# Optimization experiments

Measured on AMD Instinct MI355X. Metric: run time of the kernel, lower is better.

## Reference

```python
import jax, jax.numpy as jnp
import numpy as np

N_NODES = 100000
N_GRAPHS = 256
HIDDEN = 64
IN_DIM = 512


def gcn_conv(x, edge_index, W, b, n_nodes):
    """PyG GCNConv: out = D^{-1/2} (A+I) D^{-1/2} (x W) + b."""
    h = x @ W  # [N, H] -- transform first (as PyG does), messages are small
    src = jnp.concatenate([edge_index[0], jnp.arange(n_nodes)])  # add self loops
    dst = jnp.concatenate([edge_index[1], jnp.arange(n_nodes)])
    ones = jnp.ones(src.shape[0], dtype=h.dtype)
    deg = jax.ops.segment_sum(ones, dst, num_segments=n_nodes)
    dinv = jnp.where(deg > 0, jax.lax.rsqrt(deg), 0.0)
    norm = dinv[src] * dinv[dst]  # [E+N]
    msg = h[src] * norm[:, None]  # gather + scale
    out = jax.ops.segment_sum(msg, dst, num_segments=n_nodes)  # scatter-add
    return out + b


def global_mean_pool(x, batch, num_graphs):
    s = jax.ops.segment_sum(x, batch, num_segments=num_graphs)
    cnt = jax.ops.segment_sum(jnp.ones(x.shape[0], dtype=x.dtype), batch,
                              num_segments=num_graphs)
    return s / jnp.maximum(cnt, 1.0)[:, None]


def setup_inputs() -> dict:
    key = jax.random.key(0)
    ks = jax.random.split(key, 9)
    x = jax.random.normal(ks[0], (N_NODES, IN_DIM), dtype=jnp.float32)
    edge_index = jax.random.randint(ks[1], (2, 1600000), 0, N_NODES, dtype=jnp.int64) \
        if jax.config.jax_enable_x64 else jax.random.randint(ks[1], (2, 1600000), 0, N_NODES).astype(jnp.int32)
    batch = jnp.sort(jax.random.randint(ks[2], (N_NODES,), 0, N_GRAPHS))
    sc1 = 1.0 / np.sqrt(IN_DIM)
    sc2 = 1.0 / np.sqrt(HIDDEN)
    W1 = jax.random.uniform(ks[3], (IN_DIM, HIDDEN), minval=-sc1, maxval=sc1, dtype=jnp.float32)
    b1 = jnp.zeros((HIDDEN,), dtype=jnp.float32)
    W2 = jax.random.uniform(ks[4], (HIDDEN, HIDDEN), minval=-sc2, maxval=sc2, dtype=jnp.float32)
    b2 = jnp.zeros((HIDDEN,), dtype=jnp.float32)
    Wfc = jax.random.uniform(ks[5], (HIDDEN, 1), minval=-sc2, maxval=sc2, dtype=jnp.float32)
    bfc = jnp.zeros((1,), dtype=jnp.float32)
    return {"x": x, "edge_index": edge_index, "batch": batch,
            "W1": W1, "b1": b1, "W2": W2, "b2": b2, "Wfc": Wfc, "bfc": bfc}


def reference(x, edge_index, batch, W1, b1, W2, b2, Wfc, bfc):
    n = x.shape[0]
    h = jax.nn.relu(gcn_conv(x, edge_index, W1, b1, n))
    h = jax.nn.relu(gcn_conv(h, edge_index, W2, b2, n))
    g = global_mean_pool(h, batch, N_GRAPHS)  # [G, H]
    out = g @ Wfc + bfc  # [G, 1]
    return out.squeeze(-1)
```

## Files before the change

### kernel.cpp

```cpp
#include <hip/hip_runtime.h>

#define HIDDEN 64
#define IN_DIM 512
#define CAP 4096
#define NB_MAX 1024

typedef short v8s __attribute__((ext_vector_type(8)));
typedef float v4f __attribute__((ext_vector_type(4)));

static __device__ __forceinline__ unsigned short f2bf(float f) {
    unsigned int u = __float_as_uint(f);
    u = (u + 0x7FFF + ((u >> 16) & 1)) >> 16;
    return (unsigned short)u;
}
static __device__ __forceinline__ float bf2f(unsigned short u) {
    return __uint_as_float(((unsigned int)u) << 16);
}
static __device__ __forceinline__ float bflo(unsigned u) { return __uint_as_float(u << 16); }
static __device__ __forceinline__ float bfhi(unsigned u) { return __uint_as_float(u & 0xffff0000u); }

__global__ void k_init(int* cursor, float* gsum, int* gcnt) {
    int i = blockIdx.x * 256 + threadIdx.x;
    if (i < NB_MAX) cursor[i] = 0;
    if (i < 256) { gsum[i] = 0.f; gcnt[i] = 0; }
}

__launch_bounds__(256)
__global__ void k_bin(const int* __restrict__ src, const int* __restrict__ dst,
                      int* cursor, unsigned* __restrict__ bucket_data, int n_edges) {
    __shared__ unsigned words[4096];
    __shared__ unsigned short binsh[4096];
    __shared__ int hist[NB_MAX];
    __shared__ int base[NB_MAX];
    const int tid = threadIdx.x;
    const int e0 = blockIdx.x * 4096;
    for (int i = tid; i < NB_MAX; i += 256) hist[i] = 0;
    __syncthreads();
    for (int i = tid; i < 4096; i += 256) {
        int e = e0 + i;
        if (e < n_edges) {
            int d = dst[e], s = src[e];
            words[i] = ((unsigned)s << 7) | (unsigned)(d & 127);
            int b = d >> 7;
            binsh[i] = (unsigned short)b;
            atomicAdd(&hist[b], 1);
        } else binsh[i] = 0xFFFFu;
    }
    __syncthreads();
    for (int b = tid; b < NB_MAX; b += 256) {
        int c = hist[b];
        base[b] = c ? atomicAdd(&cursor[b], c) : 0;
        hist[b] = 0;
    }
    __syncthreads();
    for (int i = tid; i < 4096; i += 256) {
        unsigned short b = binsh[i];
        if (b != 0xFFFFu) {
            int slot = atomicAdd(&hist[b], 1);
            int p = base[b] + slot;
            if (p < CAP) bucket_data[(size_t)b * CAP + p] = words[i];
        }
    }
}

__launch_bounds__(256)
__global__ void k_bexc(const int* __restrict__ cursor, int* __restrict__ bucket_base,
                       int* __restrict__ row_start, int n_nodes, int nbuck) {
    __shared__ int wsum[4];
    const int t = threadIdx.x, lane = t & 63, w = t >> 6;
    int v[4], s = 0;
#pragma unroll
    for (int k = 0; k < 4; ++k) {
        int i = t * 4 + k;
        int c = (i < nbuck) ? cursor[i] : 0;
        if (c > CAP) c = CAP;
        v[k] = s; s += c;
    }
    int inc = s;
#pragma unroll
    for (int off = 1; off < 64; off <<= 1) {
        int u = __shfl_up(inc, off, 64);
        if (lane >= off) inc += u;
    }
    if (lane == 63) wsum[w] = inc;
    __syncthreads();
    int cross = 0;
    for (int i = 0; i < w; ++i) cross += wsum[i];
    int b0 = cross + inc - s;
#pragma unroll
    for (int k = 0; k < 4; ++k) {
        int i = t * 4 + k;
        if (i < NB_MAX) bucket_base[i] = b0 + v[k];
    }
    if (t == 255) row_start[n_nodes] = cross + inc;
}

__launch_bounds__(256)
__global__ void k_csr(const unsigned* __restrict__ bucket_data, const int* __restrict__ cursor,
                      const int* __restrict__ bucket_base,
                      int* __restrict__ row_start, int* __restrict__ csr,
                      float* __restrict__ dinv, int n_nodes) {
    __shared__ unsigned words[CAP];
    __shared__ int cnt[128];
    __shared__ int loff[128];
    __shared__ int cur[128];
    __shared__ int w0sum;
    const int tid = threadIdx.x, bin = blockIdx.x, n0 = bin << 7;
    int c = cursor[bin]; if (c > CAP) c = CAP;
    const unsigned* bd = bucket_data + (size_t)bin * CAP;
    for (int i = tid; i < c; i += 256) words[i] = bd[i];
    if (tid < 128) { cnt[tid] = 0; cur[tid] = 0; }
    __syncthreads();
    for (int i = tid; i < c; i += 256) atomicAdd(&cnt[words[i] & 127], 1);
    __syncthreads();
    int val = 0, inc = 0;
    if (tid < 128) {
        const int lane = tid & 63;
        val = cnt[tid];
        inc = val;
#pragma unroll
        for (int off = 1; off < 64; off <<= 1) {
            int u = __shfl_up(inc, off, 64);
            if (lane >= off) inc += u;
        }
        if (tid == 63) w0sum = inc;
    }
    __syncthreads();
    if (tid < 128) {
        int excl = inc - val + ((tid >= 64) ? w0sum : 0);
        loff[tid] = excl;
        int n = n0 + tid;
        if (n < n_nodes) {
            row_start[n] = bucket_base[bin] + excl;
            dinv[n] = rsqrtf((float)(val + 1));
        }
    }
    __syncthreads();
    const int gbase = bucket_base[bin];
    for (int i = tid; i < c; i += 256) {
        unsigned wd = words[i];
        int d = wd & 127;
        int slot = atomicAdd(&cur[d], 1);
        csr[gbase + loff[d] + slot] = (int)(wd >> 7);
    }
}

__global__ void k_prep(const float* __restrict__ W1, const float* __restrict__ W2,
                       unsigned short* __restrict__ Wt, unsigned short* __restrict__ Wt2) {
    int idx = blockIdx.x * 256 + threadIdx.x;
    if (idx < HIDDEN * IN_DIM) {
        int n = idx >> 9, k = idx & 511;
        Wt[(size_t)n * 512 + k] = f2bf(W1[(size_t)k * 64 + n]);
    } else {
        int j = idx - HIDDEN * IN_DIM;
        int n = j >> 6, k = j & 63;
        Wt2[(size_t)n * 64 + k] = f2bf(W2[(size_t)k * 64 + n]);
    }
}

__launch_bounds__(256)
__global__ void k_gemm1m(const float* __restrict__ x, const unsigned short* __restrict__ Wt,
                         const float* __restrict__ dinv, unsigned short* __restrict__ s1,
                         int n_nodes) {
    __shared__ __align__(16) unsigned short lX[64 * 136];
    __shared__ __align__(16) unsigned short lW[64 * 136];
    const int tid  = threadIdx.x;
    const int lane = tid & 63;
    const int w    = tid >> 6;
    const int quad = lane >> 4;
    const int m16  = lane & 15;
    const int row0 = blockIdx.x * 64;

    v4f acc[4];
#pragma unroll
    for (int b = 0; b < 4; ++b) acc[b] = (v4f){0.f, 0.f, 0.f, 0.f};

    for (int kc = 0; kc < IN_DIM; kc += 128) {
        __syncthreads();
#pragma unroll
        for (int i = 0; i < 8; ++i) {
            int fidx = tid + i * 256;
            int r  = fidx >> 5;
            int c4 = fidx & 31;
            int gr = row0 + r;
            float4 v = make_float4(0.f, 0.f, 0.f, 0.f);
            if (gr < n_nodes) v = ((const float4*)(x + (size_t)gr * IN_DIM + kc))[c4];
            ushort4 u = make_ushort4(f2bf(v.x), f2bf(v.y), f2bf(v.z), f2bf(v.w));
            *(ushort4*)(lX + r * 136 + c4 * 4) = u;
        }
#pragma unroll
        for (int i = 0; i < 4; ++i) {
            int idx = tid + i * 256;
            int n  = idx >> 4;
            int c8 = idx & 15;
            uint4 u = *(const uint4*)(Wt + (size_t)n * 512 + kc + c8 * 8);
            *(uint4*)(lW + n * 136 + c8 * 8) = u;
        }
        __syncthreads();
#pragma unroll
        for (int kk = 0; kk < 128; kk += 32) {
            v8s a = *(const v8s*)(lX + (w * 16 + m16) * 136 + kk + quad * 8);
#pragma unroll
            for (int b = 0; b < 4; ++b) {
                v8s bb = *(const v8s*)(lW + (b * 16 + m16) * 136 + kk + quad * 8);
                acc[b] = __builtin_amdgcn_mfma_f32_16x16x32_bf16(a, bb, acc[b], 0, 0, 0);
            }
        }
    }
    __syncthreads();
    float* lC = (float*)lX;
#pragma unroll
    for (int b = 0; b < 4; ++b)
#pragma unroll
        for (int r = 0; r < 4; ++r) {
            int rowt = w * 16 + quad * 4 + r;
            lC[rowt * 65 + b * 16 + m16] = acc[b][r];
        }
    __syncthreads();
#pragma unroll
    for (int i = 0; i < 2; ++i) {
        int base = i * 2048 + tid * 8;
        int r = base >> 6;
        int c = base & 63;
        int gr = row0 + r;
        if (gr < n_nodes) {
            float d = dinv[gr];
            const float* p = lC + r * 65 + c;
            unsigned p0 = (unsigned)f2bf(p[0] * d) | ((unsigned)f2bf(p[1] * d) << 16);
            unsigned p1 = (unsigned)f2bf(p[2] * d) | ((unsigned)f2bf(p[3] * d) << 16);
            unsigned p2 = (unsigned)f2bf(p[4] * d) | ((unsigned)f2bf(p[5] * d) << 16);
            unsigned p3 = (unsigned)f2bf(p[6] * d) | ((unsigned)f2bf(p[7] * d) << 16);
            *(uint4*)(s1 + (size_t)gr * 64 + c) = make_uint4(p0, p1, p2, p3);
        }
    }
}

#define NPW 4

__launch_bounds__(256)
__global__ void k_agg1(const unsigned short* __restrict__ sin, const int* __restrict__ row_start,
                       const int* __restrict__ csr, const float* __restrict__ dinv,
                       float* __restrict__ tout, int n_nodes) {
    const int tid = threadIdx.x;
    const int lane = tid & 63;
    const int wave = tid >> 6;
    const int g = lane >> 4;
    const int l = lane & 15;
    const int n0 = (blockIdx.x * 4 + wave) * NPW;
    if (n0 >= n_nodes) return;

    int rs_nxt = row_start[n0];
    int idx_nxt = csr[rs_nxt + lane];
    uint2 us_nxt = *(const uint2*)(sin + (size_t)n0 * HIDDEN + l * 4);

    for (int i = 0; i < NPW; ++i) {
        int n = n0 + i;
        if (n >= n_nodes) break;
        const int rs = rs_nxt;
        const int re = row_start[n + 1];
        const int idx = idx_nxt;
        const uint2 uself = us_nxt;
        if (i + 1 < NPW && n + 1 < n_nodes) {
            rs_nxt = re;
            idx_nxt = csr[re + lane];
            us_nxt = *(const uint2*)(sin + (size_t)(n + 1) * HIDDEN + l * 4);
        }

        float4 acc = make_float4(0.f, 0.f, 0.f, 0.f);
        int m0 = re - rs; if (m0 > 64) m0 = 64;
        int mq = (m0 + 3) >> 2;
#pragma unroll 4
        for (int jq = 0; jq < mq; ++jq) {
            int myj = jq * 4 + g;
            int cm = myj < m0 ? myj : 0;
            int a = __shfl(idx, cm, 64);
            uint2 u = *(const uint2*)(sin + (size_t)a * HIDDEN + l * 4);
            if (myj < m0) {
                acc.x += bflo(u.x); acc.y += bfhi(u.x);
                acc.z += bflo(u.y); acc.w += bfhi(u.y);
            }
        }
        if (__builtin_expect(re - rs > 64, 0)) {
            for (int base = rs + 64; base < re; base += 64) {
                int idx2 = csr[base + lane];
                int m = re - base; if (m > 64) m = 64;
                int mq2 = (m + 3) >> 2;
#pragma unroll 4
                for (int jq = 0; jq < mq2; ++jq) {
                    int myj = jq * 4 + g;
                    int cm = myj < m ? myj : 0;
                    int a = __shfl(idx2, cm, 64);
                    uint2 u = *(const uint2*)(sin + (size_t)a * HIDDEN + l * 4);
                    if (myj < m) {
                        acc.x += bflo(u.x); acc.y += bfhi(u.x);
                        acc.z += bflo(u.y); acc.w += bfhi(u.y);
                    }
                }
            }
        }
        acc.x += __shfl_xor(acc.x, 16, 64); acc.y += __shfl_xor(acc.y, 16, 64);
        acc.z += __shfl_xor(acc.z, 16, 64); acc.w += __shfl_xor(acc.w, 16, 64);
        acc.x += __shfl_xor(acc.x, 32, 64); acc.y += __shfl_xor(acc.y, 32, 64);
        acc.z += __shfl_xor(acc.z, 32, 64); acc.w += __shfl_xor(acc.w, 32, 64);
        acc.x += bflo(uself.x); acc.y += bfhi(uself.x);
        acc.z += bflo(uself.y); acc.w += bfhi(uself.y);
        float d = dinv[n];
        if (g == 0) {
            float4 t4 = make_float4(d * acc.x, d * acc.y, d * acc.z, d * acc.w);
            *(float4*)(tout + (size_t)n * HIDDEN + l * 4) = t4;
        }
    }
}

__launch_bounds__(256)
__global__ void k_gemm2m(const float* __restrict__ tin, const unsigned short* __restrict__ Wt2,
                         const float* __restrict__ b1, const float* __restrict__ dinv,
                         unsigned short* __restrict__ sout, int n_nodes) {
    __shared__ __align__(16) unsigned short lX[64 * 136];
    __shared__ __align__(16) unsigned short lW[64 * 72];
    const int tid  = threadIdx.x;
    const int lane = tid & 63;
    const int w    = tid >> 6;
    const int quad = lane >> 4;
    const int m16  = lane & 15;
    const int row0 = blockIdx.x * 64;

#pragma unroll
    for (int i = 0; i < 4; ++i) {
        int fidx = tid + i * 256;
        int r  = fidx >> 4;
        int c4 = fidx & 15;
        int gr = row0 + r;
        float4 v = make_float4(0.f, 0.f, 0.f, 0.f);
        if (gr < n_nodes) v = ((const float4*)(tin + (size_t)gr * HIDDEN))[c4];
        float4 bb = ((const float4*)b1)[c4];
        v.x = fmaxf(v.x + bb.x, 0.f);
        v.y = fmaxf(v.y + bb.y, 0.f);
        v.z = fmaxf(v.z + bb.z, 0.f);
        v.w = fmaxf(v.w + bb.w, 0.f);
        ushort4 u = make_ushort4(f2bf(v.x), f2bf(v.y), f2bf(v.z), f2bf(v.w));
        *(ushort4*)(lX + r * 72 + c4 * 4) = u;
    }
#pragma unroll
    for (int i = 0; i < 2; ++i) {
        int idx = tid + i * 256;
        int n  = idx >> 3;
        int c8 = idx & 7;
        uint4 u = *(const uint4*)(Wt2 + (size_t)n * 64 + c8 * 8);
        *(uint4*)(lW + n * 72 + c8 * 8) = u;
    }
    __syncthreads();
    v4f acc[4];
#pragma unroll
    for (int b = 0; b < 4; ++b) acc[b] = (v4f){0.f, 0.f, 0.f, 0.f};
#pragma unroll
    for (int kk = 0; kk < 64; kk += 32) {
        v8s a = *(const v8s*)(lX + (w * 16 + m16) * 72 + kk + quad * 8);
#pragma unroll
        for (int b = 0; b < 4; ++b) {
            v8s bb = *(const v8s*)(lW + (b * 16 + m16) * 72 + kk + quad * 8);
            acc[b] = __builtin_amdgcn_mfma_f32_16x16x32_bf16(a, bb, acc[b], 0, 0, 0);
        }
    }
    __syncthreads();
    float* lC = (float*)lX;
#pragma unroll
    for (int b = 0; b < 4; ++b)
#pragma unroll
        for (int r = 0; r < 4; ++r) {
            int rowt = w * 16 + quad * 4 + r;
            lC[rowt * 65 + b * 16 + m16] = acc[b][r];
        }
    __syncthreads();
#pragma unroll
    for (int i = 0; i < 2; ++i) {
        int base = i * 2048 + tid * 8;
        int r = base >> 6;
        int c = base & 63;
        int gr = row0 + r;
        if (gr < n_nodes) {
            float d = dinv[gr];
            const float* p = lC + r * 65 + c;
            unsigned p0 = (unsigned)f2bf(p[0] * d) | ((unsigned)f2bf(p[1] * d) << 16);
            unsigned p1 = (unsigned)f2bf(p[2] * d) | ((unsigned)f2bf(p[3] * d) << 16);
            unsigned p2 = (unsigned)f2bf(p[4] * d) | ((unsigned)f2bf(p[5] * d) << 16);
            unsigned p3 = (unsigned)f2bf(p[6] * d) | ((unsigned)f2bf(p[7] * d) << 16);
            *(uint4*)(sout + (size_t)gr * 64 + c) = make_uint4(p0, p1, p2, p3);
        }
    }
}

__launch_bounds__(256)
__global__ void k_layer2pool(const unsigned short* __restrict__ sin, const int* __restrict__ row_start,
                             const int* __restrict__ csr, const float* __restrict__ b2,
                             const float* __restrict__ dinv, const float* __restrict__ Wfc,
                             const int* __restrict__ batch,
                             float* gsum, int* gcnt, int n_nodes) {
    __shared__ float lsum[256];
    __shared__ int   lcnt[256];
    const int tid = threadIdx.x;
    lsum[tid] = 0.f; lcnt[tid] = 0;
    __syncthreads();
    const int lane = tid & 63;
    const int wave = tid >> 6;
    const int g = lane >> 4;
    const int l = lane & 15;
    const float4 b4  = ((const float4*)b2)[l];
    const float4 wf4 = ((const float4*)Wfc)[l];
    const int n0 = (blockIdx.x * 4 + wave) * NPW;
    if (n0 < n_nodes) {
        int rs_nxt = row_start[n0];
        int idx_nxt = csr[rs_nxt + lane];
        uint2 us_nxt = *(const uint2*)(sin + (size_t)n0 * HIDDEN + l * 4);

        for (int i = 0; i < NPW; ++i) {
            int n = n0 + i;
            if (n >= n_nodes) break;
            const int rs = rs_nxt;
            const int re = row_start[n + 1];
            const int idx = idx_nxt;
            const uint2 uself = us_nxt;
            if (i + 1 < NPW && n + 1 < n_nodes) {
                rs_nxt = re;
                idx_nxt = csr[re + lane];
                us_nxt = *(const uint2*)(sin + (size_t)(n + 1) * HIDDEN + l * 4);
            }

            float4 acc = make_float4(0.f, 0.f, 0.f, 0.f);
            int m0 = re - rs; if (m0 > 64) m0 = 64;
            int mq = (m0 + 3) >> 2;
#pragma unroll 4
            for (int jq = 0; jq < mq; ++jq) {
                int myj = jq * 4 + g;
                int cm = myj < m0 ? myj : 0;
                int a = __shfl(idx, cm, 64);
                uint2 u = *(const uint2*)(sin + (size_t)a * HIDDEN + l * 4);
                if (myj < m0) {
                    acc.x += bflo(u.x); acc.y += bfhi(u.x);
                    acc.z += bflo(u.y); acc.w += bfhi(u.y);
                }
            }
            if (__builtin_expect(re - rs > 64, 0)) {
                for (int base = rs + 64; base < re; base += 64) {
                    int idx2 = csr[base + lane];
                    int m = re - base; if (m > 64) m = 64;
                    int mq2 = (m + 3) >> 2;
#pragma unroll 4
                    for (int jq = 0; jq < mq2; ++jq) {
                        int myj = jq * 4 + g;
                        int cm = myj < m ? myj : 0;
                        int a = __shfl(idx2, cm, 64);
                        uint2 u = *(const uint2*)(sin + (size_t)a * HIDDEN + l * 4);
                        if (myj < m) {
                            acc.x += bflo(u.x); acc.y += bfhi(u.x);
                            acc.z += bflo(u.y); acc.w += bfhi(u.y);
                        }
                    }
                }
            }
            acc.x += __shfl_xor(acc.x, 16, 64); acc.y += __shfl_xor(acc.y, 16, 64);
            acc.z += __shfl_xor(acc.z, 16, 64); acc.w += __shfl_xor(acc.w, 16, 64);
            acc.x += __shfl_xor(acc.x, 32, 64); acc.y += __shfl_xor(acc.y, 32, 64);
            acc.z += __shfl_xor(acc.z, 32, 64); acc.w += __shfl_xor(acc.w, 32, 64);
            acc.x += bflo(uself.x); acc.y += bfhi(uself.x);
            acc.z += bflo(uself.y); acc.w += bfhi(uself.y);
            float d = dinv[n];
            float t = fmaxf(fmaf(d, acc.x, b4.x), 0.f) * wf4.x
                    + fmaxf(fmaf(d, acc.y, b4.y), 0.f) * wf4.y
                    + fmaxf(fmaf(d, acc.z, b4.z), 0.f) * wf4.z
                    + fmaxf(fmaf(d, acc.w, b4.w), 0.f) * wf4.w;
#pragma unroll
            for (int off = 8; off; off >>= 1) t += __shfl_down(t, off, 16);
            if (lane == 0) {
                int gr = batch[n];
                atomicAdd(&lsum[gr], t);
                atomicAdd(&lcnt[gr], 1);
            }
        }
    }
    __syncthreads();
    if (lcnt[tid]) {
        atomicAdd(&gsum[tid], lsum[tid]);
        atomicAdd(&gcnt[tid], lcnt[tid]);
    }
}

__global__ void k_out(const float* __restrict__ gsum, const int* __restrict__ gcnt,
                      const float* __restrict__ bfc, float* out) {
    int g = threadIdx.x;
    if (g < 256) {
        float c = (float)(gcnt[g] > 1 ? gcnt[g] : 1);
        out[g] = gsum[g] / c + bfc[0];
    }
}

extern "C" void kernel_launch(void* const* d_in, const int* in_sizes, int n_in,
                              void* d_out, int out_size, void* d_ws, size_t ws_size,
                              hipStream_t stream) {
    const float* x   = (const float*)d_in[0];
    const int*   ei  = (const int*)d_in[1];
    const int*   bat = (const int*)d_in[2];
    const float* W1  = (const float*)d_in[3];
    const float* b1  = (const float*)d_in[4];
    const float* W2  = (const float*)d_in[5];
    const float* b2  = (const float*)d_in[6];
    const float* Wfc = (const float*)d_in[7];
    const float* bfc = (const float*)d_in[8];
    float* out = (float*)d_out;

    const int n_nodes = in_sizes[2];
    const int n_edges = in_sizes[1] / 2;
    const int* src = ei;
    const int* dst = ei + n_edges;
    const int NBUCK = (n_nodes + 127) >> 7;

    char* w = (char*)d_ws;
    size_t off = 0;
    auto alloc = [&](size_t bytes) -> void* {
        void* p = w + off;
        off += (bytes + 255) & ~(size_t)255;
        return p;
    };
    float* dinv = (float*)alloc((size_t)n_nodes * sizeof(float));
    unsigned short* bufA = (unsigned short*)alloc((size_t)n_nodes * HIDDEN * 2);
    unsigned short* bufB = (unsigned short*)alloc((size_t)n_nodes * HIDDEN * 2);
    float* tbuf = (float*)alloc((size_t)n_nodes * HIDDEN * sizeof(float));
    unsigned short* Wt   = (unsigned short*)alloc((size_t)HIDDEN * IN_DIM * 2);
    unsigned short* Wt2  = (unsigned short*)alloc((size_t)HIDDEN * HIDDEN * 2);
    float* gsum = (float*)alloc(256 * sizeof(float));
    int*   gcnt = (int*)  alloc(256 * sizeof(int));
    int*   cursor      = (int*)alloc((size_t)NB_MAX * sizeof(int));
    int*   bucket_base = (int*)alloc((size_t)NB_MAX * sizeof(int));
    unsigned* bucket_data = (unsigned*)alloc((size_t)NB_MAX * CAP * sizeof(unsigned));
    int* row_start = (int*)alloc(((size_t)n_nodes + 1) * sizeof(int));
    int* csr       = (int*)alloc(((size_t)n_edges + 64) * sizeof(int));
    (void)ws_size; (void)n_in; (void)out_size;

    hipLaunchKernelGGL(k_init, dim3(NB_MAX / 256), dim3(256), 0, stream, cursor, gsum, gcnt);
    hipLaunchKernelGGL(k_bin, dim3((n_edges + 4095) / 4096), dim3(256), 0, stream,
                       src, dst, cursor, bucket_data, n_edges);
    hipLaunchKernelGGL(k_bexc, dim3(1), dim3(256), 0, stream,
                       cursor, bucket_base, row_start, n_nodes, NBUCK);
    hipLaunchKernelGGL(k_csr, dim3(NBUCK), dim3(256), 0, stream,
                       bucket_data, cursor, bucket_base, row_start, csr, dinv, n_nodes);
    hipLaunchKernelGGL(k_prep, dim3((HIDDEN * IN_DIM + HIDDEN * HIDDEN) / 256), dim3(256), 0, stream,
                       W1, W2, Wt, Wt2);
    hipLaunchKernelGGL(k_gemm1m, dim3((n_nodes + 63) / 64), dim3(256), 0, stream,
                       x, Wt, dinv, bufA, n_nodes);
    const int gb = (n_nodes + 4 * NPW - 1) / (4 * NPW);
    hipLaunchKernelGGL(k_agg1, dim3(gb), dim3(256), 0, stream,
                       bufA, row_start, csr, dinv, tbuf, n_nodes);
    hipLaunchKernelGGL(k_gemm2m, dim3((n_nodes + 63) / 64), dim3(256), 0, stream,
                       tbuf, Wt2, b1, dinv, bufB, n_nodes);
    hipLaunchKernelGGL(k_layer2pool, dim3(gb), dim3(256), 0, stream,
                       bufB, row_start, csr, b2, dinv, Wfc, bat, gsum, gcnt, n_nodes);
    hipLaunchKernelGGL(k_out, dim3(1), dim3(256), 0, stream, gsum, gcnt, bfc, out);
}
```

Measured before the change: 473.0 us.

## Assign one node per 16-lane group in aggregation with zero-row sentinel padding

Both aggregation kernels now map each 16-lane quarter-wave to its own destination node instead of having a whole wave walk four nodes in sequence and reduce across groups with shuffles. The CSR stores precomputed byte offsets (src<<7), and out-of-range neighbour slots point at an extra zero-filled sentinel row, so the inner loop gathers without bounds checks and is fully unrolled in chunks of 16. This removes the cross-group reductions and per-edge predication and gives more independent gathers in flight. The cost is wasted loads on padded slots for low-degree nodes and load imbalance between groups in the same wave, and the byte-offset encoding limits how large the node count can be.

```diff
diff --git a/kernel.cpp b/kernel.cpp
--- a/kernel.cpp
+++ b/kernel.cpp
@@ -19,10 +19,15 @@
 static __device__ __forceinline__ float bflo(unsigned u) { return __uint_as_float(u << 16); }
 static __device__ __forceinline__ float bfhi(unsigned u) { return __uint_as_float(u & 0xffff0000u); }
 
-__global__ void k_init(int* cursor, float* gsum, int* gcnt) {
+__global__ void k_init(int* cursor, float* gsum, int* gcnt,
+                       unsigned short* bufA, unsigned short* bufB, int n_nodes) {
     int i = blockIdx.x * 256 + threadIdx.x;
     if (i < NB_MAX) cursor[i] = 0;
     if (i < 256) { gsum[i] = 0.f; gcnt[i] = 0; }
+    if (i < 64) {
+        bufA[(size_t)n_nodes * 64 + i] = 0;
+        bufB[(size_t)n_nodes * 64 + i] = 0;
+    }
 }
 
 __launch_bounds__(256)
@@ -141,7 +146,7 @@
         unsigned wd = words[i];
         int d = wd & 127;
         int slot = atomicAdd(&cur[d], 1);
-        csr[gbase + loff[d] + slot] = (int)(wd >> 7);
+        csr[gbase + loff[d] + slot] = (int)(wd & 0xFFFFFF80u);
     }
 }
 
@@ -235,80 +240,43 @@
     }
 }
 
-#define NPW 4
-
 __launch_bounds__(256)
 __global__ void k_agg1(const unsigned short* __restrict__ sin, const int* __restrict__ row_start,
                        const int* __restrict__ csr, const float* __restrict__ dinv,
                        float* __restrict__ tout, int n_nodes) {
-    const int tid = threadIdx.x;
+    const int tid  = threadIdx.x;
     const int lane = tid & 63;
     const int wave = tid >> 6;
     const int g = lane >> 4;
     const int l = lane & 15;
-    const int n0 = (blockIdx.x * 4 + wave) * NPW;
-    if (n0 >= n_nodes) return;
-
-    int rs_nxt = row_start[n0];
-    int idx_nxt = csr[rs_nxt + lane];
-    uint2 us_nxt = *(const uint2*)(sin + (size_t)n0 * HIDDEN + l * 4);
-
-    for (int i = 0; i < NPW; ++i) {
-        int n = n0 + i;
-        if (n >= n_nodes) break;
-        const int rs = rs_nxt;
-        const int re = row_start[n + 1];
-        const int idx = idx_nxt;
-        const uint2 uself = us_nxt;
-        if (i + 1 < NPW && n + 1 < n_nodes) {
-            rs_nxt = re;
-            idx_nxt = csr[re + lane];
-            us_nxt = *(const uint2*)(sin + (size_t)(n + 1) * HIDDEN + l * 4);
-        }
-
-        float4 acc = make_float4(0.f, 0.f, 0.f, 0.f);
-        int m0 = re - rs; if (m0 > 64) m0 = 64;
-        int mq = (m0 + 3) >> 2;
-#pragma unroll 4
-        for (int jq = 0; jq < mq; ++jq) {
-            int myj = jq * 4 + g;
-            int cm = myj < m0 ? myj : 0;
-            int a = __shfl(idx, cm, 64);
-            uint2 u = *(const uint2*)(sin + (size_t)a * HIDDEN + l * 4);
-            if (myj < m0) {
-                acc.x += bflo(u.x); acc.y += bfhi(u.x);
-                acc.z += bflo(u.y); acc.w += bfhi(u.y);
-            }
-        }
-        if (__builtin_expect(re - rs > 64, 0)) {
-            for (int base = rs + 64; base < re; base += 64) {
-                int idx2 = csr[base + lane];
-                int m = re - base; if (m > 64) m = 64;
-                int mq2 = (m + 3) >> 2;
-#pragma unroll 4
-                for (int jq = 0; jq < mq2; ++jq) {
-                    int myj = jq * 4 + g;
-                    int cm = myj < m ? myj : 0;
-                    int a = __shfl(idx2, cm, 64);
-                    uint2 u = *(const uint2*)(sin + (size_t)a * HIDDEN + l * 4);
-                    if (myj < m) {
-                        acc.x += bflo(u.x); acc.y += bfhi(u.x);
-                        acc.z += bflo(u.y); acc.w += bfhi(u.y);
-                    }
-                }
-            }
-        }
-        acc.x += __shfl_xor(acc.x, 16, 64); acc.y += __shfl_xor(acc.y, 16, 64);
-        acc.z += __shfl_xor(acc.z, 16, 64); acc.w += __shfl_xor(acc.w, 16, 64);
-        acc.x += __shfl_xor(acc.x, 32, 64); acc.y += __shfl_xor(acc.y, 32, 64);
-        acc.z += __shfl_xor(acc.z, 32, 64); acc.w += __shfl_xor(acc.w, 32, 64);
-        acc.x += bflo(uself.x); acc.y += bfhi(uself.x);
-        acc.z += bflo(uself.y); acc.w += bfhi(uself.y);
+    const int n = (blockIdx.x * 4 + wave) * 4 + g;
+    const bool valid = (n < n_nodes);
+    const char* sp = (const char*)sin;
+    const int SENTB = n_nodes << 7;
+
+    int rs = 0, re = 0;
+    if (valid) { rs = row_start[n]; re = row_start[n + 1]; }
+
+    uint2 us = *(const uint2*)(sp + (size_t)(valid ? (n << 7) : SENTB) + l * 8);
+    float4 acc;
+    acc.x = bflo(us.x); acc.y = bfhi(us.x);
+    acc.z = bflo(us.y); acc.w = bfhi(us.y);
+
+    for (int base = rs; base < re; base += 16) {
+        int p = base + l;
+        int a = (p < re) ? csr[p] : SENTB;
+#pragma unroll
+        for (int j = 0; j < 16; ++j) {
+            int ab = __shfl(a, g * 16 + j, 64);
+            uint2 u = *(const uint2*)(sp + (size_t)(unsigned)ab + l * 8);
+            acc.x += bflo(u.x); acc.y += bfhi(u.x);
+            acc.z += bflo(u.y); acc.w += bfhi(u.y);
+        }
+    }
+    if (valid) {
         float d = dinv[n];
-        if (g == 0) {
-            float4 t4 = make_float4(d * acc.x, d * acc.y, d * acc.z, d * acc.w);
-            *(float4*)(tout + (size_t)n * HIDDEN + l * 4) = t4;
-        }
+        *(float4*)(tout + (size_t)n * HIDDEN + l * 4) =
+            make_float4(d * acc.x, d * acc.y, d * acc.z, d * acc.w);
     }
 }
 
@@ -405,78 +373,43 @@
     const int wave = tid >> 6;
     const int g = lane >> 4;
     const int l = lane & 15;
+    const int n = (blockIdx.x * 4 + wave) * 4 + g;
+    const bool valid = (n < n_nodes);
+    const char* sp = (const char*)sin;
+    const int SENTB = n_nodes << 7;
+
+    int rs = 0, re = 0;
+    if (valid) { rs = row_start[n]; re = row_start[n + 1]; }
+
+    uint2 us = *(const uint2*)(sp + (size_t)(valid ? (n << 7) : SENTB) + l * 8);
+    float4 acc;
+    acc.x = bflo(us.x); acc.y = bfhi(us.x);
+    acc.z = bflo(us.y); acc.w = bfhi(us.y);
+
+    for (int base = rs; base < re; base += 16) {
+        int p = base + l;
+        int a = (p < re) ? csr[p] : SENTB;
+#pragma unroll
+        for (int j = 0; j < 16; ++j) {
+            int ab = __shfl(a, g * 16 + j, 64);
+            uint2 u = *(const uint2*)(sp + (size_t)(unsigned)ab + l * 8);
+            acc.x += bflo(u.x); acc.y += bfhi(u.x);
+            acc.z += bflo(u.y); acc.w += bfhi(u.y);
+        }
+    }
+    float d = dinv[valid ? n : 0];
     const float4 b4  = ((const float4*)b2)[l];
     const float4 wf4 = ((const float4*)Wfc)[l];
-    const int n0 = (blockIdx.x * 4 + wave) * NPW;
-    if (n0 < n_nodes) {
-        int rs_nxt = row_start[n0];
-        int idx_nxt = csr[rs_nxt + lane];
-        uint2 us_nxt = *(const uint2*)(sin + (size_t)n0 * HIDDEN + l * 4);
-
-        for (int i = 0; i < NPW; ++i) {
-            int n = n0 + i;
-            if (n >= n_nodes) break;
-            const int rs = rs_nxt;
-            const int re = row_start[n + 1];
-            const int idx = idx_nxt;
-            const uint2 uself = us_nxt;
-            if (i + 1 < NPW && n + 1 < n_nodes) {
-                rs_nxt = re;
-                idx_nxt = csr[re + lane];
-                us_nxt = *(const uint2*)(sin + (size_t)(n + 1) * HIDDEN + l * 4);
-            }
-
-            float4 acc = make_float4(0.f, 0.f, 0.f, 0.f);
-            int m0 = re - rs; if (m0 > 64) m0 = 64;
-            int mq = (m0 + 3) >> 2;
-#pragma unroll 4
-            for (int jq = 0; jq < mq; ++jq) {
-                int myj = jq * 4 + g;
-                int cm = myj < m0 ? myj : 0;
-                int a = __shfl(idx, cm, 64);
-                uint2 u = *(const uint2*)(sin + (size_t)a * HIDDEN + l * 4);
-                if (myj < m0) {
-                    acc.x += bflo(u.x); acc.y += bfhi(u.x);
-                    acc.z += bflo(u.y); acc.w += bfhi(u.y);
-                }
-            }
-            if (__builtin_expect(re - rs > 64, 0)) {
-                for (int base = rs + 64; base < re; base += 64) {
-                    int idx2 = csr[base + lane];
-                    int m = re - base; if (m > 64) m = 64;
-                    int mq2 = (m + 3) >> 2;
-#pragma unroll 4
-                    for (int jq = 0; jq < mq2; ++jq) {
-                        int myj = jq * 4 + g;
-                        int cm = myj < m ? myj : 0;
-                        int a = __shfl(idx2, cm, 64);
-                        uint2 u = *(const uint2*)(sin + (size_t)a * HIDDEN + l * 4);
-                        if (myj < m) {
-                            acc.x += bflo(u.x); acc.y += bfhi(u.x);
-                            acc.z += bflo(u.y); acc.w += bfhi(u.y);
-                        }
-                    }
-                }
-            }
-            acc.x += __shfl_xor(acc.x, 16, 64); acc.y += __shfl_xor(acc.y, 16, 64);
-            acc.z += __shfl_xor(acc.z, 16, 64); acc.w += __shfl_xor(acc.w, 16, 64);
-            acc.x += __shfl_xor(acc.x, 32, 64); acc.y += __shfl_xor(acc.y, 32, 64);
-            acc.z += __shfl_xor(acc.z, 32, 64); acc.w += __shfl_xor(acc.w, 32, 64);
-            acc.x += bflo(uself.x); acc.y += bfhi(uself.x);
-            acc.z += bflo(uself.y); acc.w += bfhi(uself.y);
-            float d = dinv[n];
-            float t = fmaxf(fmaf(d, acc.x, b4.x), 0.f) * wf4.x
-                    + fmaxf(fmaf(d, acc.y, b4.y), 0.f) * wf4.y
-                    + fmaxf(fmaf(d, acc.z, b4.z), 0.f) * wf4.z
-                    + fmaxf(fmaf(d, acc.w, b4.w), 0.f) * wf4.w;
-#pragma unroll
-            for (int off = 8; off; off >>= 1) t += __shfl_down(t, off, 16);
-            if (lane == 0) {
-                int gr = batch[n];
-                atomicAdd(&lsum[gr], t);
-                atomicAdd(&lcnt[gr], 1);
-            }
-        }
+    float t = fmaxf(fmaf(d, acc.x, b4.x), 0.f) * wf4.x
+            + fmaxf(fmaf(d, acc.y, b4.y), 0.f) * wf4.y
+            + fmaxf(fmaf(d, acc.z, b4.z), 0.f) * wf4.z
+            + fmaxf(fmaf(d, acc.w, b4.w), 0.f) * wf4.w;
+#pragma unroll
+    for (int off = 8; off; off >>= 1) t += __shfl_down(t, off, 16);
+    if (l == 0 && valid) {
+        int gr = batch[n];
+        atomicAdd(&lsum[gr], t);
+        atomicAdd(&lcnt[gr], 1);
     }
     __syncthreads();
     if (lcnt[tid]) {
@@ -522,8 +455,8 @@
         return p;
     };
     float* dinv = (float*)alloc((size_t)n_nodes * sizeof(float));
-    unsigned short* bufA = (unsigned short*)alloc((size_t)n_nodes * HIDDEN * 2);
-    unsigned short* bufB = (unsigned short*)alloc((size_t)n_nodes * HIDDEN * 2);
+    unsigned short* bufA = (unsigned short*)alloc(((size_t)n_nodes + 1) * HIDDEN * 2);
+    unsigned short* bufB = (unsigned short*)alloc(((size_t)n_nodes + 1) * HIDDEN * 2);
     float* tbuf = (float*)alloc((size_t)n_nodes * HIDDEN * sizeof(float));
     unsigned short* Wt   = (unsigned short*)alloc((size_t)HIDDEN * IN_DIM * 2);
     unsigned short* Wt2  = (unsigned short*)alloc((size_t)HIDDEN * HIDDEN * 2);
@@ -536,7 +469,8 @@
     int* csr       = (int*)alloc(((size_t)n_edges + 64) * sizeof(int));
     (void)ws_size; (void)n_in; (void)out_size;
 
-    hipLaunchKernelGGL(k_init, dim3(NB_MAX / 256), dim3(256), 0, stream, cursor, gsum, gcnt);
+    hipLaunchKernelGGL(k_init, dim3(NB_MAX / 256), dim3(256), 0, stream,
+                       cursor, gsum, gcnt, bufA, bufB, n_nodes);
     hipLaunchKernelGGL(k_bin, dim3((n_edges + 4095) / 4096), dim3(256), 0, stream,
                        src, dst, cursor, bucket_data, n_edges);
     hipLaunchKernelGGL(k_bexc, dim3(1), dim3(256), 0, stream,
@@ -547,7 +481,7 @@
                        W1, W2, Wt, Wt2);
     hipLaunchKernelGGL(k_gemm1m, dim3((n_nodes + 63) / 64), dim3(256), 0, stream,
                        x, Wt, dinv, bufA, n_nodes);
-    const int gb = (n_nodes + 4 * NPW - 1) / (4 * NPW);
+    const int gb = (n_nodes + 15) / 16;
     hipLaunchKernelGGL(k_agg1, dim3(gb), dim3(256), 0, stream,
                        bufA, row_start, csr, dinv, tbuf, n_nodes);
     hipLaunchKernelGGL(k_gemm2m, dim3((n_nodes + 63) / 64), dim3(256), 0, stream,
```

Result: faster. 435.5 us (-7.9%).
